# Kernel optimization log

Measured on AMD Instinct MI355X. Metric: run time of the kernel, lower is better.

## Reference

```python
import jax, jax.numpy as jnp
import numpy as np

N, E = 50000, 800000
DIN, DH, DOUT = 128, 128, 64


def _w(k, fan_in, fan_out):
    return (jax.random.normal(k, (fan_in, fan_out), jnp.float32) / np.sqrt(fan_in)).astype(jnp.float32)


def setup_inputs() -> dict:
    key = jax.random.key(0)
    ks = jax.random.split(key, 12)
    x = jax.random.normal(ks[0], (N, DIN), jnp.float32)
    edge_index = jax.random.randint(ks[1], (2, E), 0, N, dtype=jnp.int64)
    return {
        "x": x,
        "edge_index": edge_index,
        # sage1 block: SAGEConv(DIN->DH) -> relu -> SAGEConv(DH->DH)
        "Ws11": _w(ks[2], DIN, DH), "Wn11": _w(ks[3], DIN, DH), "b11": jnp.zeros((DH,), jnp.float32),
        "Ws12": _w(ks[4], DH, DH),  "Wn12": _w(ks[5], DH, DH),  "b12": jnp.zeros((DH,), jnp.float32),
        # sage2 block: SAGEConv(DH->DH) -> relu -> SAGEConv(DH->DH)
        "Ws21": _w(ks[6], DH, DH),  "Wn21": _w(ks[7], DH, DH),  "b21": jnp.zeros((DH,), jnp.float32),
        "Ws22": _w(ks[8], DH, DH),  "Wn22": _w(ks[9], DH, DH),  "b22": jnp.zeros((DH,), jnp.float32),
        # classifier
        "Wc": _w(ks[10], DH, DOUT), "bc": jnp.zeros((DOUT,), jnp.float32),
    }


def _sage_conv(h, src, tgt, Ws, Wn, b, n):
    # mean-aggregate neighbor features (src -> tgt), then self + neighbor linear
    msgs = h[src]                                                   # [E, d] gather
    deg = jax.ops.segment_sum(jnp.ones((src.shape[0],), h.dtype), tgt, num_segments=n)
    agg = jax.ops.segment_sum(msgs, tgt, num_segments=n)
    agg = agg / jnp.maximum(deg, 1.0)[:, None]                      # [n, d]
    return h @ Ws + agg @ Wn + b


def reference(x, edge_index, Ws11, Wn11, b11, Ws12, Wn12, b12,
              Ws21, Wn21, b21, Ws22, Wn22, b22, Wc, bc):
    src, tgt = edge_index[0], edge_index[1]
    n = x.shape[0]
    # sage1 block (2 layers) + outer relu
    h = jax.nn.relu(_sage_conv(x, src, tgt, Ws11, Wn11, b11, n))
    h = _sage_conv(h, src, tgt, Ws12, Wn12, b12, n)
    h = jax.nn.relu(h)
    # dropout (eval mode): identity
    # sage2 block (2 layers) + outer relu
    h = jax.nn.relu(_sage_conv(h, src, tgt, Ws21, Wn21, b21, n))
    h = _sage_conv(h, src, tgt, Ws22, Wn22, b22, n)
    h = jax.nn.relu(h)
    # global mean pool over nodes, then classify
    g = jnp.mean(h, axis=0)                                         # [DH]
    return g @ Wc + bc                                              # [DOUT]
```

## Files before the change

kernel.cpp:

```cpp
#include <hip/hip_runtime.h>
#include <hip/hip_bf16.h>
#include <hip/hip_fp16.h>
#include <hip/hip_fp8.h>


typedef _Float16 f16x8 __attribute__((ext_vector_type(8)));
typedef float f32x4 __attribute__((ext_vector_type(4)));

__global__ __launch_bounds__(256) void k_bucket(
    const int* __restrict__ src, const int* __restrict__ tgt,
    int* __restrict__ deg8, unsigned long long* __restrict__ staging,
    int* __restrict__ bucket_fill, int E, int bdiv, int cap, int N) {
  __shared__ unsigned long long buf[8][320];
  __shared__ int cnt[8];
  __shared__ int base[8];
  int tid = threadIdx.x;
  int lane = tid & 63;
  if (tid < 8) cnt[tid] = 0;
  __syncthreads();
  int* degrep = deg8 + (size_t)(blockIdx.x & 7) * N;
  int e0 = blockIdx.x * 2048;
#pragma unroll
  for (int i = 0; i < 8; ++i) {
    int e = e0 + i * 256 + tid;
    int b = -1;
    unsigned long long pair = 0;
    if (e < E) {
      int t = tgt[e];
      int s = src[e];
      atomicAdd(&degrep[t], 1);
      b = t / bdiv;
      pair = ((unsigned long long)(unsigned)t << 32) | (unsigned)s;
    }
#pragma unroll
    for (int bk = 0; bk < 8; ++bk) {
      bool mine = (b == bk);
      unsigned long long mask = __ballot(mine);
      if (mask == 0ull) continue;
      int cw = __popcll(mask);
      int leader = __ffsll((unsigned long long)mask) - 1;
      int p0 = 0;
      if (lane == leader) p0 = atomicAdd(&cnt[bk], cw);
      p0 = __shfl(p0, leader, 64);
      if (mine) {
        int p = p0 + __popcll(mask & ((1ull << lane) - 1ull));
        if (p < 320) {
          buf[bk][p] = pair;
        } else {
          int gp = atomicAdd(&bucket_fill[bk], 1);
          staging[(size_t)bk * cap + gp] = pair;
        }
      }
    }
  }
  __syncthreads();
  if (tid < 8) {
    int c = min(cnt[tid], 320);
    base[tid] = atomicAdd(&bucket_fill[tid], c);
    cnt[tid] = c;
  }
  __syncthreads();
  for (int b = 0; b < 8; ++b) {
    int c = cnt[b];
    for (int p = tid; p < c; p += 256)
      staging[(size_t)b * cap + base[b] + p] = buf[b][p];
  }
}

__global__ __launch_bounds__(256) void k_scatter2(
    const unsigned long long* __restrict__ staging,
    const int* __restrict__ bucket_fill, int* __restrict__ cursor,
    int* __restrict__ csr_src, int cap) {
  int b = blockIdx.x & 7;
  int nchunk = gridDim.x >> 3;
  int chunk = blockIdx.x >> 3;
  int n = bucket_fill[b];
  const unsigned long long* sb = staging + (size_t)b * cap;
  for (int i0 = chunk * 2048; i0 < n; i0 += nchunk * 2048) {
#pragma unroll
    for (int t = 0; t < 8; ++t) {
      int i = i0 + t * 256 + (int)threadIdx.x;
      if (i < n) {
        unsigned long long pair = sb[i];
        int tg = (int)(pair >> 32);
        int s = (int)(pair & 0xffffffffu);
        int pos = atomicAdd(&cursor[tg], 1);
        csr_src[pos] = s;
      }
    }
  }
}

__global__ __launch_bounds__(256) void k_scan1(const int* __restrict__ deg8,
                                               int* __restrict__ partial,
                                               int* __restrict__ blocksum,
                                               float* __restrict__ inv_deg,
                                               int n) {
  __shared__ int s[256];
  int tid = threadIdx.x;
  int i = blockIdx.x * 256 + tid;
  int v = 0;
  if (i < n) {
#pragma unroll
    for (int k = 0; k < 8; ++k) v += deg8[(size_t)k * n + i];
  }
  s[tid] = v;
  __syncthreads();
  for (int off = 1; off < 256; off <<= 1) {
    int t = (tid >= off) ? s[tid - off] : 0;
    __syncthreads();
    s[tid] += t;
    __syncthreads();
  }
  if (i < n) {
    partial[i] = s[tid] - v;
    inv_deg[i] = 1.0f / fmaxf((float)v, 1.0f);
  }
  if (tid == 255) blocksum[blockIdx.x] = s[255];
}

__global__ __launch_bounds__(256) void k_scan2(int* __restrict__ blocksum, int nb) {
  __shared__ int s[256];
  int tid = threadIdx.x;
  int v = (tid < nb) ? blocksum[tid] : 0;
  s[tid] = v;
  __syncthreads();
  for (int off = 1; off < 256; off <<= 1) {
    int t = (tid >= off) ? s[tid - off] : 0;
    __syncthreads();
    s[tid] += t;
    __syncthreads();
  }
  if (tid < nb) blocksum[tid] = s[tid] - v;
}

__global__ __launch_bounds__(256) void k_scan3(const int* __restrict__ partial,
                                               const int* __restrict__ blocksum,
                                               int* __restrict__ row_start,
                                               int* __restrict__ cursor, int n, int E) {
  int i = blockIdx.x * 256 + threadIdx.x;
  if (i < n) {
    int r = partial[i] + blocksum[blockIdx.x];
    row_start[i] = r;
    cursor[i] = r;
  }
  if (i == 0) row_start[n] = E;
}

__global__ __launch_bounds__(256) void k_cvt_x(const float* __restrict__ x,
                                               __half* __restrict__ xh,
                                               unsigned char* __restrict__ xh8,
                                               int total8) {
  int i = blockIdx.x * 256 + threadIdx.x;
  if (i >= total8) return;
  const float4* p = (const float4*)(x + (size_t)i * 8);
  float4 v0 = p[0], v1 = p[1];
  float f[8] = {v0.x, v0.y, v0.z, v0.w, v1.x, v1.y, v1.z, v1.w};
  f16x8 o;
  unsigned long long u8 = 0;
#pragma unroll
  for (int j = 0; j < 8; ++j) {
    o[j] = (_Float16)f[j];
    __hip_fp8_e4m3 q(f[j]);
    u8 |= (unsigned long long)(*reinterpret_cast<unsigned char*>(&q)) << (8 * j);
  }
  *(f16x8*)(xh + (size_t)i * 8) = o;
  *(unsigned long long*)(xh8 + (size_t)i * 8) = u8;
}

struct WPack {
  const float* s[4];
  const float* n[4];
};

__global__ __launch_bounds__(256) void k_prep_w(WPack p, __half* __restrict__ Wt) {
  int l = blockIdx.y;
  int i = blockIdx.x * 256 + threadIdx.x;
  int n = i >> 8;
  int k = i & 255;
  const float* W = (k < 128) ? p.s[l] : p.n[l];
  float v = W[(size_t)(k & 127) * 128 + n];
  Wt[(size_t)l * 32768 + (size_t)n * 256 + k] = __float2half(v);
}

__global__ __launch_bounds__(256) void k_agg8(
    const unsigned char* __restrict__ h8, const int* __restrict__ csr_src,
    const int* __restrict__ row_start, const float* __restrict__ inv_deg,
    __half* __restrict__ agg, int n_nodes) {
  int gw = (blockIdx.x * 256 + (int)threadIdx.x) >> 6;
  int lane = threadIdx.x & 63;
  if (gw >= n_nodes) return;
  int q = lane >> 4;
  int dl = (lane & 15) * 8;
  int beg = row_start[gw];
  int end = row_start[gw + 1];
  __half2 ac0 = __float2half2_rn(0.f), ac1 = ac0, ac2 = ac0, ac3 = ac0;

  auto accum = [&](uint2 w) {
    unsigned v0 = w.x, v1 = w.y;
    unsigned e0 = ((v0 & 0x00800080u) << 8) | ((v0 & 0x007f007fu) << 7);
    unsigned o0 = (((v0 >> 8) & 0x00800080u) << 8) | (((v0 >> 8) & 0x007f007fu) << 7);
    unsigned e1 = ((v1 & 0x00800080u) << 8) | ((v1 & 0x007f007fu) << 7);
    unsigned o1 = (((v1 >> 8) & 0x00800080u) << 8) | (((v1 >> 8) & 0x007f007fu) << 7);
    ac0 = __hadd2(ac0, *reinterpret_cast<__half2*>(&e0));
    ac1 = __hadd2(ac1, *reinterpret_cast<__half2*>(&o0));
    ac2 = __hadd2(ac2, *reinterpret_cast<__half2*>(&e1));
    ac3 = __hadd2(ac3, *reinterpret_cast<__half2*>(&o1));
  };

  int e = beg;
  for (; e + 16 <= end; e += 16) {
    int i0 = csr_src[e + q];
    int i1 = csr_src[e + 4 + q];
    int i2 = csr_src[e + 8 + q];
    int i3 = csr_src[e + 12 + q];
    uint2 w0 = *(const uint2*)(h8 + (size_t)i0 * 128 + dl);
    uint2 w1 = *(const uint2*)(h8 + (size_t)i1 * 128 + dl);
    uint2 w2 = *(const uint2*)(h8 + (size_t)i2 * 128 + dl);
    uint2 w3 = *(const uint2*)(h8 + (size_t)i3 * 128 + dl);
    accum(w0);
    accum(w1);
    accum(w2);
    accum(w3);
  }
  for (; e + 8 <= end; e += 8) {
    int i0 = csr_src[e + q];
    int i1 = csr_src[e + 4 + q];
    uint2 w0 = *(const uint2*)(h8 + (size_t)i0 * 128 + dl);
    uint2 w1 = *(const uint2*)(h8 + (size_t)i1 * 128 + dl);
    accum(w0);
    accum(w1);
  }
  for (; e + 4 <= end; e += 4) {
    int i0 = csr_src[e + q];
    accum(*(const uint2*)(h8 + (size_t)i0 * 128 + dl));
  }
  if (e + q < end) {
    int i0 = csr_src[e + q];
    accum(*(const uint2*)(h8 + (size_t)i0 * 128 + dl));
  }
#pragma unroll
  for (int off = 16; off <= 32; off <<= 1) {
    int t0 = __shfl_xor(*reinterpret_cast<int*>(&ac0), off, 64);
    int t1 = __shfl_xor(*reinterpret_cast<int*>(&ac1), off, 64);
    int t2 = __shfl_xor(*reinterpret_cast<int*>(&ac2), off, 64);
    int t3 = __shfl_xor(*reinterpret_cast<int*>(&ac3), off, 64);
    ac0 = __hadd2(ac0, *reinterpret_cast<__half2*>(&t0));
    ac1 = __hadd2(ac1, *reinterpret_cast<__half2*>(&t1));
    ac2 = __hadd2(ac2, *reinterpret_cast<__half2*>(&t2));
    ac3 = __hadd2(ac3, *reinterpret_cast<__half2*>(&t3));
  }
  if (q == 0) {
    float wgt = inv_deg[gw] * 256.0f;
    float2 f0 = __half22float2(ac0);
    float2 f1 = __half22float2(ac1);
    float2 f2 = __half22float2(ac2);
    float2 f3 = __half22float2(ac3);
    f16x8 r;
    r[0] = (_Float16)(f0.x * wgt);
    r[1] = (_Float16)(f1.x * wgt);
    r[2] = (_Float16)(f0.y * wgt);
    r[3] = (_Float16)(f1.y * wgt);
    r[4] = (_Float16)(f2.x * wgt);
    r[5] = (_Float16)(f3.x * wgt);
    r[6] = (_Float16)(f2.y * wgt);
    r[7] = (_Float16)(f3.y * wgt);
    *(f16x8*)(agg + (size_t)gw * 128 + dl) = r;
  }
}

__global__ __launch_bounds__(256) void k_linear_mfma(
    const __half* __restrict__ h, const __half* __restrict__ agg,
    const __half* __restrict__ Wt, const float* __restrict__ bias,
    __half* __restrict__ out, unsigned char* __restrict__ out8, int n_nodes) {
  int tid = threadIdx.x;
  int cq = tid >> 6;
  int lane = tid & 63;
  int node0 = blockIdx.x * 64;
  int lr = lane & 15;
  int lg = lane >> 4;

  f16x8 bs[8][2];
#pragma unroll
  for (int ks = 0; ks < 8; ++ks) {
    int kb = ks * 32 + lg * 8;
    bs[ks][0] = *(const f16x8*)(Wt + (size_t)(cq * 32 + lr) * 256 + kb);
    bs[ks][1] = *(const f16x8*)(Wt + (size_t)(cq * 32 + 16 + lr) * 256 + kb);
  }

  f32x4 acc[4][2];
#pragma unroll
  for (int rt = 0; rt < 4; ++rt)
#pragma unroll
    for (int ct = 0; ct < 2; ++ct) acc[rt][ct] = (f32x4){0.f, 0.f, 0.f, 0.f};

  const __half* hrow[4];
  const __half* grow[4];
#pragma unroll
  for (int rt = 0; rt < 4; ++rt) {
    int arow = node0 + rt * 16 + lr;
    if (arow >= n_nodes) arow = n_nodes - 1;
    hrow[rt] = h + (size_t)arow * 128;
    grow[rt] = agg + (size_t)arow * 128;
  }

#pragma unroll
  for (int ks = 0; ks < 8; ++ks) {
    int koff = (ks & 3) * 32 + lg * 8;
#pragma unroll
    for (int rt = 0; rt < 4; ++rt) {
      f16x8 a = (ks < 4) ? *(const f16x8*)(hrow[rt] + koff)
                         : *(const f16x8*)(grow[rt] + koff);
      acc[rt][0] = __builtin_amdgcn_mfma_f32_16x16x32_f16(a, bs[ks][0], acc[rt][0], 0, 0, 0);
      acc[rt][1] = __builtin_amdgcn_mfma_f32_16x16x32_f16(a, bs[ks][1], acc[rt][1], 0, 0, 0);
    }
  }

#pragma unroll
  for (int ct = 0; ct < 2; ++ct) {
    int n_col = cq * 32 + ct * 16 + lr;
    float bv = bias[n_col];
#pragma unroll
    for (int rt = 0; rt < 4; ++rt) {
#pragma unroll
      for (int r = 0; r < 4; ++r) {
        int m = node0 + rt * 16 + lg * 4 + r;
        if (m < n_nodes) {
          float v = fmaxf(acc[rt][ct][r] + bv, 0.f);
          out[(size_t)m * 128 + n_col] = __float2half(v);
          if (out8) {
            __hip_fp8_e4m3 q(v);
            out8[(size_t)m * 128 + n_col] = *reinterpret_cast<unsigned char*>(&q);
          }
        }
      }
    }
  }
}

__global__ __launch_bounds__(256) void k_pool(const __half* __restrict__ h,
                                              float* __restrict__ partial, int n_nodes) {
  __shared__ float red[4][128];
  int tid = threadIdx.x;
  int lane = tid & 63;
  int w = tid >> 6;
  float a0 = 0.f, a1 = 0.f;
  for (int n = blockIdx.x * 4 + w; n < n_nodes; n += gridDim.x * 4) {
    float2 f = __half22float2(*(const __half2*)(h + (size_t)n * 128 + lane * 2));
    a0 += f.x;
    a1 += f.y;
  }
  red[w][lane * 2] = a0;
  red[w][lane * 2 + 1] = a1;
  __syncthreads();
  if (tid < 128) {
    partial[(size_t)blockIdx.x * 128 + tid] =
        (red[0][tid] + red[1][tid]) + (red[2][tid] + red[3][tid]);
  }
}

__global__ __launch_bounds__(512) void k_final(const float* __restrict__ partial,
                                               const float* __restrict__ Wc,
                                               const float* __restrict__ bc,
                                               float* __restrict__ out, int n_nodes) {
  __shared__ float red[4][128];
  __shared__ float gs[128];
  __shared__ float red2[8][64];
  int tid = threadIdx.x;
  int j = tid & 127;
  int c = tid >> 7;
  float s = 0.f;
#pragma unroll
  for (int b = 0; b < 64; ++b) s += partial[(size_t)(c * 64 + b) * 128 + j];
  red[c][j] = s;
  __syncthreads();
  if (tid < 128) {
    float g = (red[0][tid] + red[1][tid]) + (red[2][tid] + red[3][tid]);
    gs[tid] = g / (float)n_nodes;
  }
  __syncthreads();
  {
    int jo = tid & 63;
    int c2 = tid >> 6;
    float s2 = 0.f;
#pragma unroll
    for (int d = 0; d < 16; ++d)
      s2 += gs[c2 * 16 + d] * Wc[(size_t)(c2 * 16 + d) * 64 + jo];
    red2[c2][jo] = s2;
  }
  __syncthreads();
  if (tid < 64) {
    float o = bc[tid];
#pragma unroll
    for (int c2 = 0; c2 < 8; ++c2) o += red2[c2][tid];
    out[tid] = o;
  }
}

extern "C" void kernel_launch(void* const* d_in, const int* in_sizes, int n_in,
                              void* d_out, int out_size, void* d_ws, size_t ws_size,
                              hipStream_t stream) {
  const float* x = (const float*)d_in[0];
  const int* ei = (const int*)d_in[1];
  const float* Ws11 = (const float*)d_in[2];
  const float* Wn11 = (const float*)d_in[3];
  const float* b11 = (const float*)d_in[4];
  const float* Ws12 = (const float*)d_in[5];
  const float* Wn12 = (const float*)d_in[6];
  const float* b12 = (const float*)d_in[7];
  const float* Ws21 = (const float*)d_in[8];
  const float* Wn21 = (const float*)d_in[9];
  const float* b21 = (const float*)d_in[10];
  const float* Ws22 = (const float*)d_in[11];
  const float* Wn22 = (const float*)d_in[12];
  const float* b22 = (const float*)d_in[13];
  const float* Wc = (const float*)d_in[14];
  const float* bc = (const float*)d_in[15];

  int N = in_sizes[0] / 128;
  int E = in_sizes[1] / 2;
  const int* src = ei;
  const int* tgt = ei + E;

  int bdiv = (N + 7) / 8;
  int cap = E / 8 + 8192;

  char* w = (char*)d_ws;
  size_t off = 0;
  auto alloc = [&](size_t bytes) {
    void* p = w + off;
    off += (bytes + 255) & ~(size_t)255;
    return p;
  };
  __half* xh = (__half*)alloc((size_t)N * 128 * 2);
  __half* hA = (__half*)alloc((size_t)N * 128 * 2);
  __half* hB = (__half*)alloc((size_t)N * 128 * 2);
  __half* aggb = (__half*)alloc((size_t)N * 128 * 2);
  unsigned char* xh8 = (unsigned char*)alloc((size_t)N * 128);
  unsigned char* h8A = (unsigned char*)alloc((size_t)N * 128);
  unsigned char* h8B = (unsigned char*)alloc((size_t)N * 128);
  __half* Wt = (__half*)alloc((size_t)4 * 32768 * 2);
  float* partial = (float*)alloc((size_t)256 * 128 * 4);
  float* inv_deg = (float*)alloc((size_t)N * 4);
  int* deg8 = (int*)alloc((size_t)8 * N * 4);
  int* row_start = (int*)alloc((size_t)(N + 1) * 4);
  int* cursor = (int*)alloc((size_t)N * 4);
  int* csr_src = (int*)alloc((size_t)E * 4);
  int* scanp = (int*)alloc((size_t)N * 4);
  int* blocksum = (int*)alloc((size_t)256 * 4);
  unsigned long long* staging =
      (unsigned long long*)alloc((size_t)8 * cap * 8);
  int* bucket_fill = (int*)alloc((size_t)8 * 4);

  hipMemsetAsync(deg8, 0, (size_t)8 * N * 4, stream);
  hipMemsetAsync(bucket_fill, 0, 8 * 4, stream);
  hipMemsetAsync(partial, 0, (size_t)256 * 128 * 4, stream);

  int nb = (N + 255) / 256;
  int bb = (E + 2047) / 2048;
  k_bucket<<<bb, 256, 0, stream>>>(src, tgt, deg8, staging, bucket_fill, E, bdiv, cap, N);
  k_scan1<<<nb, 256, 0, stream>>>(deg8, scanp, blocksum, inv_deg, N);
  k_scan2<<<1, 256, 0, stream>>>(blocksum, nb);
  k_scan3<<<nb, 256, 0, stream>>>(scanp, blocksum, row_start, cursor, N, E);
  k_scatter2<<<448, 256, 0, stream>>>(staging, bucket_fill, cursor, csr_src, cap);

  int total8 = N * 128 / 8;
  int cb = (total8 + 255) / 256;
  k_cvt_x<<<cb, 256, 0, stream>>>(x, xh, xh8, total8);
  WPack wp;
  wp.s[0] = Ws11; wp.s[1] = Ws12; wp.s[2] = Ws21; wp.s[3] = Ws22;
  wp.n[0] = Wn11; wp.n[1] = Wn12; wp.n[2] = Wn21; wp.n[3] = Wn22;
  k_prep_w<<<dim3(128, 4), 256, 0, stream>>>(wp, Wt);

  int ab = (N + 3) / 4;
  int lb = (N + 63) / 64;

  k_agg8<<<ab, 256, 0, stream>>>(xh8, csr_src, row_start, inv_deg, aggb, N);
  k_linear_mfma<<<lb, 256, 0, stream>>>(xh, aggb, Wt + 0 * 32768, b11, hA, h8A, N);
  k_agg8<<<ab, 256, 0, stream>>>(h8A, csr_src, row_start, inv_deg, aggb, N);
  k_linear_mfma<<<lb, 256, 0, stream>>>(hA, aggb, Wt + 1 * 32768, b12, hB, h8B, N);
  k_agg8<<<ab, 256, 0, stream>>>(h8B, csr_src, row_start, inv_deg, aggb, N);
  k_linear_mfma<<<lb, 256, 0, stream>>>(hB, aggb, Wt + 2 * 32768, b21, hA, h8A, N);
  k_agg8<<<ab, 256, 0, stream>>>(h8A, csr_src, row_start, inv_deg, aggb, N);
  k_linear_mfma<<<lb, 256, 0, stream>>>(hA, aggb, Wt + 3 * 32768, b22, hB, (unsigned char*)nullptr, N);

  k_pool<<<256, 256, 0, stream>>>(hB, partial, N);
  k_final<<<1, 512, 0, stream>>>(partial, Wc, bc, (float*)d_out, N);
}
```

Baseline: 334.7 us.

## Widen aggregation gathers to 16-byte loads and merge workspace memsets

The fp8 neighbour-aggregation kernel now has each lane load 16 bytes (uint4) of a source row, so 8 lanes cover a row and each wave processes 8 edges per step instead of 4. This halves the number of gather instructions and cuts one shuffle-reduction stage per accumulator, at the cost of twice as many accumulator registers and more per-lane unpacking work. Separately, the workspace buffers that need zeroing (deg8, bucket_fill, partial) are placed next to each other so a single memset clears them, replacing three memset calls.

```diff
diff --git a/kernel.cpp b/kernel.cpp
--- a/kernel.cpp
+++ b/kernel.cpp
@@ -190,82 +190,70 @@
   int gw = (blockIdx.x * 256 + (int)threadIdx.x) >> 6;
   int lane = threadIdx.x & 63;
   if (gw >= n_nodes) return;
-  int q = lane >> 4;
-  int dl = (lane & 15) * 8;
+  int slot = lane >> 3;
+  int dl = (lane & 7) * 16;
   int beg = row_start[gw];
   int end = row_start[gw + 1];
-  __half2 ac0 = __float2half2_rn(0.f), ac1 = ac0, ac2 = ac0, ac3 = ac0;
-
-  auto accum = [&](uint2 w) {
-    unsigned v0 = w.x, v1 = w.y;
-    unsigned e0 = ((v0 & 0x00800080u) << 8) | ((v0 & 0x007f007fu) << 7);
-    unsigned o0 = (((v0 >> 8) & 0x00800080u) << 8) | (((v0 >> 8) & 0x007f007fu) << 7);
-    unsigned e1 = ((v1 & 0x00800080u) << 8) | ((v1 & 0x007f007fu) << 7);
-    unsigned o1 = (((v1 >> 8) & 0x00800080u) << 8) | (((v1 >> 8) & 0x007f007fu) << 7);
-    ac0 = __hadd2(ac0, *reinterpret_cast<__half2*>(&e0));
-    ac1 = __hadd2(ac1, *reinterpret_cast<__half2*>(&o0));
-    ac2 = __hadd2(ac2, *reinterpret_cast<__half2*>(&e1));
-    ac3 = __hadd2(ac3, *reinterpret_cast<__half2*>(&o1));
+  __half2 ac[8];
+#pragma unroll
+  for (int j = 0; j < 8; ++j) ac[j] = __float2half2_rn(0.f);
+
+  auto accum = [&](uint4 w) {
+    unsigned v[4] = {w.x, w.y, w.z, w.w};
+#pragma unroll
+    for (int j = 0; j < 4; ++j) {
+      unsigned ev = ((v[j] & 0x00800080u) << 8) | ((v[j] & 0x007f007fu) << 7);
+      unsigned od = (((v[j] >> 8) & 0x00800080u) << 8) | (((v[j] >> 8) & 0x007f007fu) << 7);
+      ac[2 * j] = __hadd2(ac[2 * j], *reinterpret_cast<__half2*>(&ev));
+      ac[2 * j + 1] = __hadd2(ac[2 * j + 1], *reinterpret_cast<__half2*>(&od));
+    }
   };
 
   int e = beg;
   for (; e + 16 <= end; e += 16) {
-    int i0 = csr_src[e + q];
-    int i1 = csr_src[e + 4 + q];
-    int i2 = csr_src[e + 8 + q];
-    int i3 = csr_src[e + 12 + q];
-    uint2 w0 = *(const uint2*)(h8 + (size_t)i0 * 128 + dl);
-    uint2 w1 = *(const uint2*)(h8 + (size_t)i1 * 128 + dl);
-    uint2 w2 = *(const uint2*)(h8 + (size_t)i2 * 128 + dl);
-    uint2 w3 = *(const uint2*)(h8 + (size_t)i3 * 128 + dl);
+    int i0 = csr_src[e + slot];
+    int i1 = csr_src[e + 8 + slot];
+    uint4 w0 = *(const uint4*)(h8 + (size_t)i0 * 128 + dl);
+    uint4 w1 = *(const uint4*)(h8 + (size_t)i1 * 128 + dl);
     accum(w0);
     accum(w1);
-    accum(w2);
-    accum(w3);
   }
   for (; e + 8 <= end; e += 8) {
-    int i0 = csr_src[e + q];
-    int i1 = csr_src[e + 4 + q];
-    uint2 w0 = *(const uint2*)(h8 + (size_t)i0 * 128 + dl);
-    uint2 w1 = *(const uint2*)(h8 + (size_t)i1 * 128 + dl);
-    accum(w0);
-    accum(w1);
-  }
-  for (; e + 4 <= end; e += 4) {
-    int i0 = csr_src[e + q];
-    accum(*(const uint2*)(h8 + (size_t)i0 * 128 + dl));
-  }
-  if (e + q < end) {
-    int i0 = csr_src[e + q];
-    accum(*(const uint2*)(h8 + (size_t)i0 * 128 + dl));
-  }
-#pragma unroll
-  for (int off = 16; off <= 32; off <<= 1) {
-    int t0 = __shfl_xor(*reinterpret_cast<int*>(&ac0), off, 64);
-    int t1 = __shfl_xor(*reinterpret_cast<int*>(&ac1), off, 64);
-    int t2 = __shfl_xor(*reinterpret_cast<int*>(&ac2), off, 64);
-    int t3 = __shfl_xor(*reinterpret_cast<int*>(&ac3), off, 64);
-    ac0 = __hadd2(ac0, *reinterpret_cast<__half2*>(&t0));
-    ac1 = __hadd2(ac1, *reinterpret_cast<__half2*>(&t1));
-    ac2 = __hadd2(ac2, *reinterpret_cast<__half2*>(&t2));
-    ac3 = __hadd2(ac3, *reinterpret_cast<__half2*>(&t3));
-  }
-  if (q == 0) {
+    int i0 = csr_src[e + slot];
+    accum(*(const uint4*)(h8 + (size_t)i0 * 128 + dl));
+  }
+  if (e + slot < end) {
+    int i0 = csr_src[e + slot];
+    accum(*(const uint4*)(h8 + (size_t)i0 * 128 + dl));
+  }
+#pragma unroll
+  for (int off = 8; off <= 32; off <<= 1) {
+#pragma unroll
+    for (int j = 0; j < 8; ++j) {
+      int t = __shfl_xor(*reinterpret_cast<int*>(&ac[j]), off, 64);
+      ac[j] = __hadd2(ac[j], *reinterpret_cast<__half2*>(&t));
+    }
+  }
+  if (slot == 0) {
     float wgt = inv_deg[gw] * 256.0f;
-    float2 f0 = __half22float2(ac0);
-    float2 f1 = __half22float2(ac1);
-    float2 f2 = __half22float2(ac2);
-    float2 f3 = __half22float2(ac3);
-    f16x8 r;
-    r[0] = (_Float16)(f0.x * wgt);
-    r[1] = (_Float16)(f1.x * wgt);
-    r[2] = (_Float16)(f0.y * wgt);
-    r[3] = (_Float16)(f1.y * wgt);
-    r[4] = (_Float16)(f2.x * wgt);
-    r[5] = (_Float16)(f3.x * wgt);
-    r[6] = (_Float16)(f2.y * wgt);
-    r[7] = (_Float16)(f3.y * wgt);
-    *(f16x8*)(agg + (size_t)gw * 128 + dl) = r;
+    f16x8 r0, r1;
+#pragma unroll
+    for (int j = 0; j < 4; ++j) {
+      float2 fe = __half22float2(ac[2 * j]);
+      float2 fo = __half22float2(ac[2 * j + 1]);
+      _Float16 d0 = (_Float16)(fe.x * wgt);
+      _Float16 d1 = (_Float16)(fo.x * wgt);
+      _Float16 d2 = (_Float16)(fe.y * wgt);
+      _Float16 d3 = (_Float16)(fo.y * wgt);
+      if (j < 2) {
+        r0[4 * j] = d0; r0[4 * j + 1] = d1; r0[4 * j + 2] = d2; r0[4 * j + 3] = d3;
+      } else {
+        r1[4 * (j - 2)] = d0; r1[4 * (j - 2) + 1] = d1;
+        r1[4 * (j - 2) + 2] = d2; r1[4 * (j - 2) + 3] = d3;
+      }
+    }
+    *(f16x8*)(agg + (size_t)gw * 128 + dl) = r0;
+    *(f16x8*)(agg + (size_t)gw * 128 + dl + 8) = r1;
   }
 }
 
@@ -440,9 +428,12 @@
   unsigned char* h8A = (unsigned char*)alloc((size_t)N * 128);
   unsigned char* h8B = (unsigned char*)alloc((size_t)N * 128);
   __half* Wt = (__half*)alloc((size_t)4 * 32768 * 2);
+  float* inv_deg = (float*)alloc((size_t)N * 4);
+  size_t zbase = off;
+  int* deg8 = (int*)alloc((size_t)8 * N * 4);
+  int* bucket_fill = (int*)alloc((size_t)8 * 4);
   float* partial = (float*)alloc((size_t)256 * 128 * 4);
-  float* inv_deg = (float*)alloc((size_t)N * 4);
-  int* deg8 = (int*)alloc((size_t)8 * N * 4);
+  size_t zbytes = off - zbase;
   int* row_start = (int*)alloc((size_t)(N + 1) * 4);
   int* cursor = (int*)alloc((size_t)N * 4);
   int* csr_src = (int*)alloc((size_t)E * 4);
@@ -450,11 +441,8 @@
   int* blocksum = (int*)alloc((size_t)256 * 4);
   unsigned long long* staging =
       (unsigned long long*)alloc((size_t)8 * cap * 8);
-  int* bucket_fill = (int*)alloc((size_t)8 * 4);
-
-  hipMemsetAsync(deg8, 0, (size_t)8 * N * 4, stream);
-  hipMemsetAsync(bucket_fill, 0, 8 * 4, stream);
-  hipMemsetAsync(partial, 0, (size_t)256 * 128 * 4, stream);
+
+  hipMemsetAsync((char*)d_ws + zbase, 0, zbytes, stream);
 
   int nb = (N + 255) / 256;
   int bb = (E + 2047) / 2048;
```

Result: no change. 333.0 us (-0.5%).
